# Kernel optimization log

Measured on AMD Instinct MI355X. Metric: run time of the kernel, lower is better.

Reference implementation:

```python
import jax, jax.numpy as jnp
import numpy as np
import math

H = 16
LORA_SCALING = 16 / 8  # alpha / r
NEG_INF = -1e30

def _alibi_slopes(n_heads):
    start = 2.0 ** (-(2.0 ** (-(math.log2(n_heads) - 3))))
    return jnp.asarray([start * start ** i for i in range(n_heads)], dtype=jnp.float32)

def setup_inputs() -> dict:
    key = jax.random.key(0)
    ks = jax.random.split(key, 11)
    B, T, E, r = 4, 2048, 1024, 8
    d = {
        'x':  jax.random.normal(ks[0], (B, T, E), jnp.float32),
        'Wq': jax.random.normal(ks[1], (E, E), jnp.float32) * (E ** -0.5),
        'Aq': jax.random.normal(ks[2], (E, r), jnp.float32) * 0.01,
        'Bq': jax.random.normal(ks[3], (r, E), jnp.float32) * 0.01,
        'Wk': jax.random.normal(ks[4], (E, E), jnp.float32) * (E ** -0.5),
        'Ak': jax.random.normal(ks[5], (E, r), jnp.float32) * 0.01,
        'Bk': jax.random.normal(ks[6], (r, E), jnp.float32) * 0.01,
        'Wv': jax.random.normal(ks[7], (E, E), jnp.float32) * (E ** -0.5),
        'Av': jax.random.normal(ks[8], (E, r), jnp.float32) * 0.01,
        'Bv': jax.random.normal(ks[9], (r, E), jnp.float32) * 0.01,
        'Wp': jax.random.normal(ks[10], (E, E), jnp.float32) * (E ** -0.5),
    }
    return d

def _lora(x, W, A, Bm):
    # nn.Linear: x @ W.T ; LoRA: x @ B.T @ A.T * scaling
    return x @ W.T + ((x @ Bm.T) @ A.T) * LORA_SCALING

def reference(x, Wq, Aq, Bq, Wk, Ak, Bk, Wv, Av, Bv, Wp):
    B, T, E = x.shape
    dh = E // H
    q = _lora(x, Wq, Aq, Bq).reshape(B, T, H, dh).transpose(0, 2, 1, 3)  # [B,H,T,dh]
    k = _lora(x, Wk, Ak, Bk).reshape(B, T, H, dh).transpose(0, 2, 1, 3)
    v = _lora(x, Wv, Av, Bv).reshape(B, T, H, dh).transpose(0, 2, 1, 3)
    s = jnp.einsum('bhqd,bhkd->bhqk', q, k) / jnp.sqrt(jnp.float32(dh))
    i = jnp.arange(T)[:, None]
    j = jnp.arange(T)[None, :]
    slopes = _alibi_slopes(H)
    bias = slopes[:, None, None] * (i - j).astype(jnp.float32)  # [H,T,T]
    s = s + bias[None]
    s = jnp.where(j[None, None] <= i[None, None], s, NEG_INF)  # causal mask
    out = jnp.einsum('bhqk,bhkd->bhqd', jax.nn.softmax(s, axis=-1), v)
    out = out.transpose(0, 2, 1, 3).reshape(B, T, E)
    return out @ Wp.T  # dropout is identity in eval
```

## Files before the change

### kernel.cpp

```cpp
#include <hip/hip_runtime.h>

typedef unsigned short u16;
typedef unsigned int u32;
typedef u16  u16x8 __attribute__((ext_vector_type(8)));
typedef u16  u16x4 __attribute__((ext_vector_type(4)));
typedef u32  u32x4 __attribute__((ext_vector_type(4)));
typedef __bf16 bf16x2 __attribute__((ext_vector_type(2)));
typedef __bf16 bf16x8 __attribute__((ext_vector_type(8)));
typedef float f32x4 __attribute__((ext_vector_type(4)));
typedef float f32x16 __attribute__((ext_vector_type(16)));

__constant__ int KBW[16]  = {0,1,1,2,3,5,7,10,14,20,28,40,56,80,113,160};

__constant__ unsigned char RANKTBL[256] = {
  0xBF,0xCF,0xDF,0xEF,0xFF,
  0xBE,0xCE,0xDE,0xEE,0xFE,
  0xAE,0xAF,
  0xAD,0xBD,0xCD,0xDD,0xED,0xFD,
  0xAC,0xBC,0xCC,0xDC,0xEC,0xFC,
  0xAB,0xBB,0xCB,0xDB,0xEB,0xFB,
  0xAA,0xBA,0xCA,0xDA,0xEA,0xFA,
  0x9A,0x9B,0x9C,0x9D,0x9E,0x9F,
  0x99,0xA9,0xB9,0xC9,0xD9,0xE9,0xF9,
  0x98,0xA8,0xB8,0xC8,0xD8,0xE8,0xF8,
  0x97,0xA7,0xB7,0xC7,0xD7,0xE7,0xF7,
  0x87,0x88,0x89,0x8A,0x8B,0x8C,0x8D,0x8E,0x8F,
  0x86,0x96,0xA6,0xB6,0xC6,0xD6,0xE6,0xF6,
  0x85,0x95,0xA5,0xB5,0xC5,0xD5,0xE5,0xF5,
  0x75,0x76,0x77,0x78,0x79,0x7A,0x7B,0x7C,0x7D,0x7E,0x7F,
  0x74,0x84,0x94,0xA4,0xB4,0xC4,0xD4,0xE4,0xF4,
  0x63,0x64,0x65,0x66,0x67,0x68,0x69,0x6A,0x6B,0x6C,0x6D,0x6E,0x6F,
  0x73,0x83,0x93,0xA3,0xB3,0xC3,0xD3,0xE3,0xF3,
  0x52,0x53,0x54,0x55,0x56,0x57,0x58,0x59,0x5A,0x5B,0x5C,0x5D,0x5E,0x5F,
  0x62,0x72,0x82,0x92,0xA2,0xB2,0xC2,0xD2,0xE2,0xF2,
  0x41,0x42,0x43,0x44,0x45,0x46,0x47,0x48,0x49,0x4A,0x4B,0x4C,0x4D,0x4E,0x4F,
  0x51,0x61,0x71,0x81,0x91,0xA1,0xB1,0xC1,0xD1,0xE1,0xF1,
  0x31,0x32,0x33,0x34,0x35,0x36,0x37,0x38,0x39,0x3A,0x3B,0x3C,0x3D,0x3E,0x3F,
  0x10,0x11,0x12,0x13,0x14,0x15,0x16,0x17,0x18,0x19,0x1A,0x1B,0x1C,0x1D,0x1E,0x1F,
  0x20,0x21,0x22,0x23,0x24,0x25,0x26,0x27,0x28,0x29,0x2A,0x2B,0x2C,0x2D,0x2E,0x2F,
  0x30,0x40,0x50,0x60,0x70,0x80,0x90,0xA0,0xB0,0xC0,0xD0,0xE0,0xF0,
  0x00,0x01,0x02,0x03,0x04,0x05,0x06,0x07,0x08,0x09,0x0A,0x0B,0x0C,0x0D,0x0E,0x0F
};

static __device__ __forceinline__ u16 f2bf(float f) {
  unsigned int u = __float_as_uint(f);
  u += 0x7FFFu + ((u >> 16) & 1u);
  return (u16)(u >> 16);
}

static __device__ __forceinline__ u32 packbf(float a, float b) {
  bf16x2 t;
  t[0] = (__bf16)a;
  t[1] = (__bf16)b;
  return __builtin_bit_cast(u32, t);
}

static __device__ __forceinline__ f32x4 mfma16(bf16x8 a, bf16x8 b, f32x4 c) {
  return __builtin_amdgcn_mfma_f32_16x16x32_bf16(a, b, c, 0, 0, 0);
}
static __device__ __forceinline__ f32x16 mfma32(bf16x8 a, bf16x8 b, f32x16 c) {
  return __builtin_amdgcn_mfma_f32_32x32x16_bf16(a, b, c, 0, 0, 0);
}

static __device__ __forceinline__ void gload16(const void* g, void* lds) {
  __builtin_amdgcn_global_load_lds(
      (const __attribute__((address_space(1))) unsigned int*)g,
      (__attribute__((address_space(3))) unsigned int*)lds, 16, 0, 0);
}

__global__ __launch_bounds__(256) void k_cast_x(const float* __restrict__ in,
                                                u16* __restrict__ out) {
  size_t i = (size_t)blockIdx.x * 256 + threadIdx.x;
  const float4* p = reinterpret_cast<const float4*>(in) + i * 2;
  float4 a = p[0], b = p[1];
  u16x8 r;
  r[0] = f2bf(a.x); r[1] = f2bf(a.y); r[2] = f2bf(a.z); r[3] = f2bf(a.w);
  r[4] = f2bf(b.x); r[5] = f2bf(b.y); r[6] = f2bf(b.z); r[7] = f2bf(b.w);
  *reinterpret_cast<u16x8*>(out + i * 8) = r;
}

__global__ __launch_bounds__(256) void k_fold_w(
    const float* __restrict__ Wq, const float* __restrict__ Aq, const float* __restrict__ Bq,
    const float* __restrict__ Wk, const float* __restrict__ Ak, const float* __restrict__ Bk,
    const float* __restrict__ Wv, const float* __restrict__ Av, const float* __restrict__ Bv,
    const float* __restrict__ Wp, u16* __restrict__ wqkv, u16* __restrict__ wp) {
  int n = blockIdx.x;
  int widx = n >> 10, nr = n & 1023;
  const float *W, *A, *Bm; u16* dst;
  if (widx == 0)      { W = Wq; A = Aq; Bm = Bq; dst = wqkv; }
  else if (widx == 1) { W = Wk; A = Ak; Bm = Bk; dst = wqkv + (1 << 20); }
  else if (widx == 2) { W = Wv; A = Av; Bm = Bv; dst = wqkv + (2 << 20); }
  else                { W = Wp; A = nullptr; Bm = nullptr; dst = wp; }
  int e0 = threadIdx.x * 4;
  float4 w = *reinterpret_cast<const float4*>(W + (size_t)nr * 1024 + e0);
  if (widx < 3) {
    float acx = 0.f, acy = 0.f, acz = 0.f, acw = 0.f;
#pragma unroll
    for (int r = 0; r < 8; r++) {
      float ar = A[nr * 8 + r];
      float4 bm = *reinterpret_cast<const float4*>(Bm + (size_t)r * 1024 + e0);
      acx += ar * bm.x; acy += ar * bm.y; acz += ar * bm.z; acw += ar * bm.w;
    }
    w.x += 2.0f * acx; w.y += 2.0f * acy; w.z += 2.0f * acz; w.w += 2.0f * acw;
  }
  u16x4 r4; r4[0] = f2bf(w.x); r4[1] = f2bf(w.y); r4[2] = f2bf(w.z); r4[3] = f2bf(w.w);
  *reinterpret_cast<u16x4*>(dst + (size_t)nr * 1024 + e0) = r4;
}

template<int OUTF32>
__global__ __launch_bounds__(512) void k_gemm8(const u16* __restrict__ Ag,
                                               const u16* __restrict__ Bg,
                                               void* __restrict__ C,
                                               int K, int N, int lda, int gx) {
  __shared__ __align__(16) u16 As[2][8192];
  __shared__ __align__(16) u16 Bs[2][16384];
  const int tid = threadIdx.x;
  const int wid = tid >> 6, lane = tid & 63;
  const int l15 = lane & 15, lg = lane >> 4;
  const int wr = wid >> 2, wc = wid & 3;
  const int nwg = gridDim.x, cpx = nwg >> 3;
  const int bid = (int)blockIdx.x;
  const int sid = (bid & 7) * cpx + (bid >> 3);
  const int m0 = (sid % gx) * 128, n0 = (sid / gx) * 256;

  const int lrow = lane >> 3;
  const int lslot = lane & 7;

  f32x4 acc[4][4];
#pragma unroll
  for (int i = 0; i < 4; i++)
#pragma unroll
    for (int j = 0; j < 4; j++) acc[i][j] = (f32x4)0.0f;

  auto stageA = [&](int d, int t) {
#pragma unroll
    for (int i = 0; i < 2; i++) {
      int row = i * 64 + wid * 8 + lrow;
      int sc = (lslot ^ (row & 7)) << 3;
      gload16(Ag + (size_t)(m0 + row) * lda + t * 64 + sc,
              &As[d][(i * 64 + wid * 8) * 64]);
    }
  };
  auto stageB = [&](int d, int t) {
#pragma unroll
    for (int i = 0; i < 4; i++) {
      int row = i * 64 + wid * 8 + lrow;
      int sc = (lslot ^ (row & 7)) << 3;
      gload16(Bg + (size_t)(n0 + row) * K + t * 64 + sc,
              &Bs[d][(i * 64 + wid * 8) * 64]);
    }
  };
  auto ldsA = [&](int d, int m, int kk) {
    int rr = wr * 64 + m * 16 + l15;
    return *reinterpret_cast<const bf16x8*>(&As[d][rr * 64 + (((kk * 4 + lg) ^ (rr & 7)) << 3)]);
  };
  auto ldsB = [&](int d, int n, int kk) {
    int rr = wc * 64 + n * 16 + l15;
    return *reinterpret_cast<const bf16x8*>(&Bs[d][rr * 64 + (((kk * 4 + lg) ^ (rr & 7)) << 3)]);
  };

#define MIDBAR do { asm volatile("s_barrier" ::: "memory"); \
                    asm volatile("s_waitcnt lgkmcnt(0)" ::: "memory"); } while (0)
#define ENDBAR asm volatile("s_barrier" ::: "memory")

  stageB(0, 0); stageA(0, 0); stageA(1, 1);
  asm volatile("s_waitcnt vmcnt(2)" ::: "memory");
  asm volatile("s_barrier" ::: "memory");

  bf16x8 fa[4][2], fb[2][2];
  const int nt = K >> 6;
  for (int t = 0; t < nt; ++t) {
    const int d = t & 1;
#pragma unroll
    for (int m = 0; m < 4; m++)
#pragma unroll
      for (int kk = 0; kk < 2; kk++) fa[m][kk] = ldsA(d, m, kk);
#pragma unroll
    for (int n = 0; n < 2; n++)
#pragma unroll
      for (int kk = 0; kk < 2; kk++) fb[n][kk] = ldsB(d, n, kk);
    if (t + 1 < nt) stageB(d ^ 1, t + 1);
    MIDBAR;
    __builtin_amdgcn_s_setprio(1);
#pragma unroll
    for (int m = 0; m < 4; m++)
#pragma unroll
      for (int n = 0; n < 2; n++)
#pragma unroll
        for (int kk = 0; kk < 2; kk++)
          acc[m][n] = mfma16(fa[m][kk], fb[n][kk], acc[m][n]);
    __builtin_amdgcn_s_setprio(0);
    ENDBAR;
#pragma unroll
    for (int n = 0; n < 2; n++)
#pragma unroll
      for (int kk = 0; kk < 2; kk++) fb[n][kk] = ldsB(d, n + 2, kk);
    if (t + 2 < nt) stageA(d, t + 2);
    MIDBAR;
    __builtin_amdgcn_s_setprio(1);
#pragma unroll
    for (int m = 0; m < 4; m++)
#pragma unroll
      for (int n = 0; n < 2; n++)
#pragma unroll
        for (int kk = 0; kk < 2; kk++)
          acc[m][n + 2] = mfma16(fa[m][kk], fb[n][kk], acc[m][n + 2]);
    __builtin_amdgcn_s_setprio(0);
    if (t + 2 < nt) asm volatile("s_waitcnt vmcnt(2)" ::: "memory");
    else            asm volatile("s_waitcnt vmcnt(0)" ::: "memory");
    ENDBAR;
  }
#undef MIDBAR
#undef ENDBAR

  const int rbase = m0 + wr * 64, cbase = n0 + wc * 64;
#pragma unroll
  for (int m = 0; m < 4; m++)
#pragma unroll
    for (int n = 0; n < 4; n++)
#pragma unroll
      for (int j = 0; j < 4; j++) {
        int r  = rbase + m * 16 + lg * 4 + j;
        int cc = cbase + n * 16 + l15;
        if constexpr (OUTF32) {
          reinterpret_cast<float*>(C)[(size_t)r * N + cc] = acc[m][n][j];
        } else {
          reinterpret_cast<u16*>(C)[(size_t)r * N + cc] = f2bf(acc[m][n][j]);
        }
      }
}

__global__ __launch_bounds__(256) void k_vt(const u16* __restrict__ qkv,
                                            u16* __restrict__ vt) {
  __shared__ __align__(16) u16 tile[64 * 64];
  const int tb = blockIdx.x, h = blockIdx.y, b = blockIdx.z;
  const int tid = threadIdx.x;
  const size_t rb = (size_t)b * 2048;
  const int hv = 2048 + h * 64;
#pragma unroll
  for (int p = 0; p < 2; p++) {
    int r = p * 32 + (tid >> 3);
    int c = (tid & 7) * 8;
    u16x8 v = *reinterpret_cast<const u16x8*>(qkv + (rb + tb * 64 + r) * 3072 + hv + c);
    int slot = (c >> 3) ^ (r & 7) ^ ((r >> 3) & 7);
    *reinterpret_cast<u16x8*>(tile + r * 64 + slot * 8) = v;
  }
  __syncthreads();
#pragma unroll
  for (int p = 0; p < 2; p++) {
    int d = p * 32 + (tid >> 3);
    int t0 = (tid & 7) * 8;
    u16x8 v;
#pragma unroll
    for (int j = 0; j < 8; j++) {
      int r = t0 + j;
      int slot = (d >> 3) ^ (r & 7) ^ ((r >> 3) & 7);
      v[j] = tile[r * 64 + slot * 8 + (d & 7)];
    }
    *reinterpret_cast<u16x8*>(vt + ((size_t)(b * 16 + h) * 64 + d) * 2048 + tb * 64 + t0) = v;
  }
}

__global__ __launch_bounds__(256) void k_attn(const u16* __restrict__ qkv,
                                              const u16* __restrict__ vt,
                                              u16* __restrict__ aout) {
  __shared__ __align__(16) u16 Kl[2][64 * 64];
  __shared__ __align__(16) u16 Vl[2][64 * 64];
  const int tid = threadIdx.x, wave = tid >> 6, lane = tid & 63;
  const int l31 = lane & 31, half = lane >> 5;
  const int i = (int)blockIdx.x;
  const int b = i & 3, p = i >> 2;
  const int k4 = p >> 6, j4 = p & 63;
  const int ridx = (k4 == 0) ? j4 : (k4 == 1) ? 127 - j4 : (k4 == 2) ? 128 + j4 : 255 - j4;
  const int hqv = RANKTBL[ridx];
  const int h = hqv >> 4, qb = hqv & 15;
  const int rb = b * 2048;
  const int hq = h * 64, hk = 1024 + h * 64;
  const int bh64 = (b * 16 + h) * 64;
  const int qB = qb * 128;
  const int q0w = qB + wave * 32;
  const int q = q0w + l31;

  bf16x8 qf[4];
#pragma unroll
  for (int c = 0; c < 4; c++)
    qf[c] = *reinterpret_cast<const bf16x8*>(qkv + (size_t)(rb + q) * 3072 + hq + c * 16 + half * 8);

  const float slope2 = exp2f(-0.5f * (float)(h + 1)) * 1.44269504f;
  const float c0 = 0.18033688f;

  const int kend = min(2 * qb + 1, KBW[h]);

  float mrun = -1e30f, lrun = 0.f;
  f32x16 o0 = (f32x16)0.0f, o1 = (f32x16)0.0f;

  auto stage = [&](int kvr, int dst) {
#pragma unroll
    for (int i2 = 0; i2 < 2; i2++) {
      int row = (i2 * 4 + wave) * 8 + (lane >> 3);
      int scol = ((lane & 7) ^ (row & 7)) << 3;
      gload16(qkv + (size_t)(rb + kvr + row) * 3072 + hk + scol, &Kl[dst][(i2 * 4 + wave) * 512]);
      gload16(vt + (size_t)(bh64 + row) * 2048 + kvr + scol,     &Vl[dst][(i2 * 4 + wave) * 512]);
    }
  };

  stage(0, 0);
  __syncthreads();

  int bfi = 0;
  for (int kb = 0; kb <= kend; ++kb, bfi ^= 1) {
    const int kvr = kb * 64;
    if (kb < kend) stage(kvr + 64, bfi ^ 1);

    if (kvr <= q0w + 31) {
      f32x16 s[2];
#pragma unroll
      for (int t = 0; t < 2; t++) s[t] = (f32x16)0.0f;
      __builtin_amdgcn_s_setprio(1);
#pragma unroll
      for (int t = 0; t < 2; t++) {
        int r = t * 32 + l31;
#pragma unroll
        for (int cc = 0; cc < 4; cc++) {
          bf16x8 kf = *reinterpret_cast<const bf16x8*>(
              &Kl[bfi][r * 64 + (((cc * 2 + half) ^ (r & 7)) << 3)]);
          s[t] = mfma32(kf, qf[cc], s[t]);
        }
      }
      __builtin_amdgcn_s_setprio(0);

      const bool domask = (kvr + 63 > q0w);
      const int qrel = q - kvr - half * 4;
      const float qb0 = slope2 * (float)qrel;
      const float qb1 = qb0 - slope2 * 32.0f;
      float mt = -1e30f;
      if (domask) {
#pragma unroll
        for (int t = 0; t < 2; t++) {
          const float qbt = t ? qb1 : qb0;
          const int qmt = t ? (qrel - 32) : qrel;
#pragma unroll
          for (int r = 0; r < 16; r++) {
            const int krel = (r & 3) + 8 * (r >> 2);
            float val = fmaf(s[t][r], c0, fmaf(-slope2, (float)krel, qbt));
            val = (krel <= qmt) ? val : -3.0e38f;
            s[t][r] = val;
            mt = fmaxf(mt, val);
          }
        }
      } else {
#pragma unroll
        for (int t = 0; t < 2; t++) {
          const float qbt = t ? qb1 : qb0;
#pragma unroll
          for (int r = 0; r < 16; r += 2) {
            const int k0 = (r & 3) + 8 * (r >> 2);
            const int k1 = ((r + 1) & 3) + 8 * ((r + 1) >> 2);
            float v0 = fmaf(s[t][r],     c0, fmaf(-slope2, (float)k0, qbt));
            float v1 = fmaf(s[t][r + 1], c0, fmaf(-slope2, (float)k1, qbt));
            s[t][r] = v0; s[t][r + 1] = v1;
            mt = fmaxf(mt, fmaxf(v0, v1));
          }
        }
      }
      mt = fmaxf(mt, __shfl_xor(mt, 32));

      if (__any(mt - mrun > 8.0f)) {
        float mn = fmaxf(mrun, mt);
        float al = exp2f(mrun - mn);
        mrun = mn; lrun *= al;
#pragma unroll
        for (int r = 0; r < 16; r++) { o0[r] *= al; o1[r] *= al; }
      }

      float rs0 = 0.f, rs1 = 0.f;
#pragma unroll
      for (int t = 0; t < 2; t++)
#pragma unroll
        for (int r = 0; r < 16; r++) {
          float pp = exp2f(s[t][r] - mrun);
          s[t][r] = pp;
          if (t) rs1 += pp; else rs0 += pp;
        }
      float rs = rs0 + rs1;
      rs += __shfl_xor(rs, 32);
      lrun += rs;

      bf16x8 pf[4];
#pragma unroll
      for (int t = 0; t < 2; t++)
#pragma unroll
        for (int hs = 0; hs < 2; hs++) {
          u32 A0 = packbf(s[t][8 * hs + 0], s[t][8 * hs + 1]);
          u32 B0 = packbf(s[t][8 * hs + 2], s[t][8 * hs + 3]);
          u32 C0 = packbf(s[t][8 * hs + 4], s[t][8 * hs + 5]);
          u32 D0 = packbf(s[t][8 * hs + 6], s[t][8 * hs + 7]);
          asm volatile("v_permlane32_swap_b32 %0, %1" : "+v"(A0), "+v"(C0));
          asm volatile("v_permlane32_swap_b32 %0, %1" : "+v"(B0), "+v"(D0));
          u32x4 fr; fr[0] = A0; fr[1] = B0; fr[2] = C0; fr[3] = D0;
          pf[t * 2 + hs] = __builtin_bit_cast(bf16x8, fr);
        }

      __builtin_amdgcn_s_setprio(1);
#pragma unroll
      for (int dblk = 0; dblk < 2; dblk++) {
        int r = dblk * 32 + l31;
#pragma unroll
        for (int kc = 0; kc < 4; kc++) {
          bf16x8 vf = *reinterpret_cast<const bf16x8*>(
              &Vl[bfi][r * 64 + (((kc * 2 + half) ^ (r & 7)) << 3)]);
          if (dblk) o1 = mfma32(vf, pf[kc], o1);
          else      o0 = mfma32(vf, pf[kc], o0);
        }
      }
      __builtin_amdgcn_s_setprio(0);
    }
    __syncthreads();
  }

  const float linv = 1.0f / lrun;
#pragma unroll
  for (int dblk = 0; dblk < 2; dblk++)
#pragma unroll
    for (int rg = 0; rg < 4; rg++) {
      int d0 = dblk * 32 + 8 * rg + 4 * half;
      u16x4 r4;
#pragma unroll
      for (int j = 0; j < 4; j++) {
        float v = (dblk ? o1[rg * 4 + j] : o0[rg * 4 + j]) * linv;
        r4[j] = f2bf(v);
      }
      *reinterpret_cast<u16x4*>(aout + (size_t)(rb + q) * 3072 + hq + d0) = r4;
    }
}

extern "C" void kernel_launch(void* const* d_in, const int* in_sizes, int n_in,
                              void* d_out, int out_size, void* d_ws, size_t ws_size,
                              hipStream_t stream) {
  (void)in_sizes; (void)n_in; (void)out_size; (void)ws_size;
  const float* x  = (const float*)d_in[0];
  const float* Wq = (const float*)d_in[1];
  const float* Aq = (const float*)d_in[2];
  const float* Bq = (const float*)d_in[3];
  const float* Wk = (const float*)d_in[4];
  const float* Ak = (const float*)d_in[5];
  const float* Bk = (const float*)d_in[6];
  const float* Wv = (const float*)d_in[7];
  const float* Av = (const float*)d_in[8];
  const float* Bv = (const float*)d_in[9];
  const float* Wp = (const float*)d_in[10];

  char* ws = (char*)d_ws;
  u16* xb   = (u16*)(ws);
  u16* wqkv = (u16*)(ws + 16777216);
  u16* wp   = (u16*)(ws + 23068672);
  u16* qkv  = (u16*)(ws + 25165824);
  u16* vt   = xb;
  float* out = (float*)d_out;

  k_cast_x<<<dim3(4096), dim3(256), 0, stream>>>(x, xb);
  k_fold_w<<<dim3(4096), dim3(256), 0, stream>>>(Wq, Aq, Bq, Wk, Ak, Bk, Wv, Av, Bv, Wp, wqkv, wp);
  k_gemm8<0><<<dim3(768), dim3(512), 0, stream>>>(xb, wqkv, (void*)qkv, 1024, 3072, 1024, 64);
  k_vt<<<dim3(32, 16, 4), dim3(256), 0, stream>>>(qkv, vt);
  k_attn<<<dim3(1024), dim3(256), 0, stream>>>(qkv, vt, qkv);
  k_gemm8<1><<<dim3(256), dim3(512), 0, stream>>>(qkv, wp, (void*)out, 1024, 1024, 3072, 64);
}
```

Baseline: 182.6 us.

## Use 256x256 output tiles for the QKV projection GEMM

Adds a new GEMM kernel with 256x256 block tiles (each wave computes 128x64) and uses it for the QKV projection, halving the grid from 768 to 384 blocks. Each block loads A and B once per K-step for twice as many outputs, which cuts global and LDS traffic per FLOP. The K-loop interleaves LDS fragment reads, async global prefetch and MFMA phases behind barriers. In exchange it uses more LDS (64KB), more accumulator registers, and fewer blocks, which may leave some of the 256 CUs idle in the tail.

```diff
diff --git a/kernel.cpp b/kernel.cpp
--- a/kernel.cpp
+++ b/kernel.cpp
@@ -108,6 +108,145 @@
 }
 
 template<int OUTF32>
+__global__ __launch_bounds__(512) void k_gemm256(const u16* __restrict__ Ag,
+                                                 const u16* __restrict__ Bg,
+                                                 void* __restrict__ C,
+                                                 int K, int N, int lda, int gx) {
+  __shared__ __align__(16) u16 As[2][16384];
+  __shared__ __align__(16) u16 Bs[2][16384];
+  const int tid = threadIdx.x;
+  const int wid = tid >> 6, lane = tid & 63;
+  const int l15 = lane & 15, lg = lane >> 4;
+  const int wr = wid >> 2, wc = wid & 3;
+  const int nwg = gridDim.x, cpx = nwg >> 3;
+  const int bid = (int)blockIdx.x;
+  const int sid = (bid & 7) * cpx + (bid >> 3);
+  const int m0 = (sid % gx) * 256, n0 = (sid / gx) * 256;
+
+  const int lrow = lane >> 3;
+  const int lslot = lane & 7;
+
+  f32x4 acc[8][4];
+#pragma unroll
+  for (int i = 0; i < 8; i++)
+#pragma unroll
+    for (int j = 0; j < 4; j++) acc[i][j] = (f32x4)0.0f;
+
+  auto stA = [&](int d, int t, int i) {
+    int row = i * 64 + wid * 8 + lrow;
+    int sc = (lslot ^ (row & 7)) << 3;
+    gload16(Ag + (size_t)(m0 + row) * lda + t * 64 + sc, &As[d][(i * 64 + wid * 8) * 64]);
+  };
+  auto stB = [&](int d, int t, int i) {
+    int row = i * 64 + wid * 8 + lrow;
+    int sc = (lslot ^ (row & 7)) << 3;
+    gload16(Bg + (size_t)(n0 + row) * K + t * 64 + sc, &Bs[d][(i * 64 + wid * 8) * 64]);
+  };
+  auto ldsA = [&](int d, int m, int kk) {
+    int rr = wr * 128 + m * 16 + l15;
+    return *reinterpret_cast<const bf16x8*>(&As[d][rr * 64 + (((kk * 4 + lg) ^ (rr & 7)) << 3)]);
+  };
+  auto ldsB = [&](int d, int n, int kk) {
+    int rr = wc * 64 + n * 16 + l15;
+    return *reinterpret_cast<const bf16x8*>(&Bs[d][rr * 64 + (((kk * 4 + lg) ^ (rr & 7)) << 3)]);
+  };
+
+#define MIDBAR do { asm volatile("s_barrier" ::: "memory"); \
+                    asm volatile("s_waitcnt lgkmcnt(0)" ::: "memory"); } while (0)
+#define ENDBAR asm volatile("s_barrier" ::: "memory")
+
+  stA(0, 0, 0); stA(0, 0, 1); stA(0, 0, 2); stA(0, 0, 3);
+  stB(0, 0, 0); stB(0, 0, 1); stB(0, 0, 2); stB(0, 0, 3);
+  asm volatile("s_waitcnt vmcnt(0)" ::: "memory");
+  asm volatile("s_barrier" ::: "memory");
+
+  bf16x8 fa[4][2], fbA[2][2], fbB[2][2];
+  const int nt = K >> 6;
+  for (int t = 0; t < nt; ++t) {
+    const int d = t & 1;
+    const bool st = (t + 1 < nt);
+#pragma unroll
+    for (int m = 0; m < 4; m++)
+#pragma unroll
+      for (int kk = 0; kk < 2; kk++) fa[m][kk] = ldsA(d, m, kk);
+#pragma unroll
+    for (int n = 0; n < 2; n++)
+#pragma unroll
+      for (int kk = 0; kk < 2; kk++) fbA[n][kk] = ldsB(d, n, kk);
+    if (st) { stA(d ^ 1, t + 1, 0); stA(d ^ 1, t + 1, 1); }
+    MIDBAR;
+    __builtin_amdgcn_s_setprio(1);
+#pragma unroll
+    for (int m = 0; m < 4; m++)
+#pragma unroll
+      for (int n = 0; n < 2; n++)
+#pragma unroll
+        for (int kk = 0; kk < 2; kk++)
+          acc[m][n] = mfma16(fa[m][kk], fbA[n][kk], acc[m][n]);
+    __builtin_amdgcn_s_setprio(0);
+    ENDBAR;
+#pragma unroll
+    for (int n = 0; n < 2; n++)
+#pragma unroll
+      for (int kk = 0; kk < 2; kk++) fbB[n][kk] = ldsB(d, n + 2, kk);
+    if (st) { stA(d ^ 1, t + 1, 2); stA(d ^ 1, t + 1, 3); }
+    MIDBAR;
+    __builtin_amdgcn_s_setprio(1);
+#pragma unroll
+    for (int m = 0; m < 4; m++)
+#pragma unroll
+      for (int n = 0; n < 2; n++)
+#pragma unroll
+        for (int kk = 0; kk < 2; kk++)
+          acc[m][n + 2] = mfma16(fa[m][kk], fbB[n][kk], acc[m][n + 2]);
+    __builtin_amdgcn_s_setprio(0);
+    ENDBAR;
+#pragma unroll
+    for (int m = 0; m < 4; m++)
+#pragma unroll
+      for (int kk = 0; kk < 2; kk++) fa[m][kk] = ldsA(d, m + 4, kk);
+    if (st) { stB(d ^ 1, t + 1, 0); stB(d ^ 1, t + 1, 1); stB(d ^ 1, t + 1, 2); stB(d ^ 1, t + 1, 3); }
+    MIDBAR;
+    __builtin_amdgcn_s_setprio(1);
+#pragma unroll
+    for (int m = 0; m < 4; m++)
+#pragma unroll
+      for (int n = 0; n < 2; n++)
+#pragma unroll
+        for (int kk = 0; kk < 2; kk++)
+          acc[m + 4][n + 2] = mfma16(fa[m][kk], fbB[n][kk], acc[m + 4][n + 2]);
+#pragma unroll
+    for (int m = 0; m < 4; m++)
+#pragma unroll
+      for (int n = 0; n < 2; n++)
+#pragma unroll
+        for (int kk = 0; kk < 2; kk++)
+          acc[m + 4][n] = mfma16(fa[m][kk], fbA[n][kk], acc[m + 4][n]);
+    __builtin_amdgcn_s_setprio(0);
+    asm volatile("s_waitcnt vmcnt(0)" ::: "memory");
+    ENDBAR;
+  }
+#undef MIDBAR
+#undef ENDBAR
+
+  const int rbase = m0 + wr * 128, cbase = n0 + wc * 64;
+#pragma unroll
+  for (int m = 0; m < 8; m++)
+#pragma unroll
+    for (int n = 0; n < 4; n++)
+#pragma unroll
+      for (int j = 0; j < 4; j++) {
+        int r  = rbase + m * 16 + lg * 4 + j;
+        int cc = cbase + n * 16 + l15;
+        if constexpr (OUTF32) {
+          reinterpret_cast<float*>(C)[(size_t)r * N + cc] = acc[m][n][j];
+        } else {
+          reinterpret_cast<u16*>(C)[(size_t)r * N + cc] = f2bf(acc[m][n][j]);
+        }
+      }
+}
+
+template<int OUTF32>
 __global__ __launch_bounds__(512) void k_gemm8(const u16* __restrict__ Ag,
                                                const u16* __restrict__ Bg,
                                                void* __restrict__ C,
@@ -460,7 +599,7 @@
 
   k_cast_x<<<dim3(4096), dim3(256), 0, stream>>>(x, xb);
   k_fold_w<<<dim3(4096), dim3(256), 0, stream>>>(Wq, Aq, Bq, Wk, Ak, Bk, Wv, Av, Bv, Wp, wqkv, wp);
-  k_gemm8<0><<<dim3(768), dim3(512), 0, stream>>>(xb, wqkv, (void*)qkv, 1024, 3072, 1024, 64);
+  k_gemm256<0><<<dim3(384), dim3(512), 0, stream>>>(xb, wqkv, (void*)qkv, 1024, 3072, 1024, 32);
   k_vt<<<dim3(32, 16, 4), dim3(256), 0, stream>>>(qkv, vt);
   k_attn<<<dim3(1024), dim3(256), 0, stream>>>(qkv, vt, qkv);
   k_gemm8<1><<<dim3(256), dim3(512), 0, stream>>>(qkv, wp, (void*)out, 1024, 1024, 3072, 64);
```

Measured after the change: 180.7 us. Within noise of the previous version (-1.1%).
